# Kernel tuning notes

Measured on AMD Instinct MI355X. Metric: run time of the kernel, lower is better.

Reference implementation:

```python
import jax, jax.numpy as jnp
import numpy as np

N_CODE, PC = 127, 63
LENGTH = N_CODE + PC          # 190
D_MODEL, D_STATE, D_CONV, EXPAND = 512, 16, 4, 2
D_INNER = EXPAND * D_MODEL    # 1024
DT_RANK = (D_MODEL + 15) // 16  # 32
BATCH = 16


def _build_mask(pcm):
    # faithful translation of build_mask(code)
    L = N_CODE + PC
    mask = np.eye(L, dtype=np.float64)
    for r in range(PC):
        idx = np.where(pcm[r] > 0)[0]
        for jj in idx:
            for kk in idx:
                if jj != kk:
                    mask[jj, kk] += 1
                    mask[kk, jj] += 1
                    mask[N_CODE + r, jj] += 1
                    mask[jj, N_CODE + r] += 1
    return mask > 0


def setup_inputs() -> dict:
    rng = np.random.default_rng(0)
    # LDPC-like sparse parity-check matrix, row weight 6
    pcm = np.zeros((PC, N_CODE), np.int32)
    for r in range(PC):
        pcm[r, rng.choice(N_CODE, 6, replace=False)] = 1
    pc_mask = jnp.asarray(_build_mask(pcm))

    def w(shape, fan_in):
        return jnp.asarray((rng.standard_normal(shape) / np.sqrt(fan_in)).astype(np.float32))

    inp = {
        "x": jnp.asarray(rng.standard_normal((BATCH, LENGTH, D_MODEL)).astype(np.float32)),
        "pc_mask": pc_mask,
        # masked resize linears (torch Linear: y = x @ W.T + b)
        "in_resize_w": w((LENGTH, D_MODEL), D_MODEL),
        "in_resize_b": jnp.zeros((LENGTH,), jnp.float32),
        "in_reset_w": w((D_MODEL, LENGTH), LENGTH),
        "in_reset_b": jnp.zeros((D_MODEL,), jnp.float32),
        "out_resize_w": w((LENGTH, D_MODEL), D_MODEL),
        "out_resize_b": jnp.zeros((LENGTH,), jnp.float32),
        "out_reset_w": w((D_MODEL, LENGTH), LENGTH),
        "out_reset_b": jnp.zeros((D_MODEL,), jnp.float32),
        # Mamba block params
        "in_proj_w": w((2 * D_INNER, D_MODEL), D_MODEL),
        "conv_w": w((D_INNER, D_CONV), D_CONV),          # depthwise conv kernels
        "conv_b": jnp.zeros((D_INNER,), jnp.float32),
        "x_proj_w": w((DT_RANK + 2 * D_STATE, D_INNER), D_INNER),
        "dt_proj_w": w((D_INNER, DT_RANK), DT_RANK),
        "dt_proj_b": jnp.full((D_INNER,), -4.6, jnp.float32),  # softplus ~ 0.01
        "A_log": jnp.log(jnp.tile(jnp.arange(1, D_STATE + 1, dtype=jnp.float32), (D_INNER, 1))),
        "D": jnp.ones((D_INNER,), jnp.float32),
        "out_proj_w": w((D_MODEL, D_INNER), D_INNER),
        # LayerNorm over (length, d_model)
        "norm_w": jnp.ones((LENGTH, D_MODEL), jnp.float32),
        "norm_b": jnp.zeros((LENGTH, D_MODEL), jnp.float32),
    }
    return inp


def _forward(x, pc_mask, in_resize_w, in_resize_b, in_reset_w, in_reset_b,
             out_resize_w, out_resize_b, out_reset_w, out_reset_b,
             in_proj_w, conv_w, conv_b, x_proj_w, dt_proj_w, dt_proj_b,
             A_log, D, out_proj_w, norm_w, norm_b):
    dt_rank = dt_proj_w.shape[1]
    d_state = A_log.shape[1]
    d_conv = conv_w.shape[1]

    def mamba(h):
        # h: [B, L, d_model]
        xz = h @ in_proj_w.T                       # [B, L, 2*d_inner]
        xc, z = jnp.split(xz, 2, axis=-1)
        # depthwise causal conv along L
        xt = xc.transpose(0, 2, 1)                 # [B, d_inner, L]
        xt = jax.lax.conv_general_dilated(
            xt, conv_w[:, None, :], (1,), [(d_conv - 1, 0)],
            dimension_numbers=("NCH", "OIH", "NCH"),
            feature_group_count=xt.shape[1])
        xc = jax.nn.silu((xt + conv_b[None, :, None]).transpose(0, 2, 1))  # [B,L,di]
        x_dbl = xc @ x_proj_w.T                    # [B, L, dt_rank+2*ds]
        dt = jax.nn.softplus(x_dbl[..., :dt_rank] @ dt_proj_w.T + dt_proj_b)
        Bm = x_dbl[..., dt_rank:dt_rank + d_state]  # [B, L, ds]
        Cm = x_dbl[..., dt_rank + d_state:]         # [B, L, ds]
        A = -jnp.exp(A_log)                         # [di, ds]
        dA = jnp.exp(dt[..., None] * A)             # [B, L, di, ds]
        dBu = (dt * xc)[..., None] * Bm[:, :, None, :]

        def step(hst, inp):
            a, b = inp
            hst = a * hst + b
            return hst, hst

        h0 = jnp.zeros((dA.shape[0], dA.shape[2], dA.shape[3]), dA.dtype)
        _, hs = jax.lax.scan(step, h0, (dA.transpose(1, 0, 2, 3), dBu.transpose(1, 0, 2, 3)))
        y = jnp.einsum("lbds,bls->bld", hs, Cm) + xc * D
        return (y * jax.nn.silu(z)) @ out_proj_w.T  # [B, L, d_model]

    m = pc_mask.astype(x.dtype)
    h = (x @ in_resize_w.T + in_resize_b) * m[0, 0]
    h = (h @ in_reset_w.T + in_reset_b) * x
    o = mamba(h) + jnp.flip(mamba(jnp.flip(h, 1)), 1)  # bidirectional scan
    o = (o @ out_resize_w.T + out_resize_b) * m        # [B,L,L] * [L,L]
    o = (o @ out_reset_w.T + out_reset_b) * x
    # LayerNorm over last two dims (length, d_model)
    t = jnp.tanh(x)
    mu = jnp.mean(t, axis=(-2, -1), keepdims=True)
    var = jnp.var(t, axis=(-2, -1), keepdims=True)
    out = (t - mu) * jax.lax.rsqrt(var + 1e-5) * norm_w + norm_b
    # original module returns only `out`; `o` is also returned here to keep the
    # (otherwise dead) bidirectional selective-scan path observable.
    return out, o


def reference(x, pc_mask, in_resize_w, in_resize_b, in_reset_w, in_reset_b,
              out_resize_w, out_resize_b, out_reset_w, out_reset_b,
              in_proj_w, conv_w, conv_b, x_proj_w, dt_proj_w, dt_proj_b,
              A_log, D, out_proj_w, norm_w, norm_b):
    return _forward(x, pc_mask, in_resize_w, in_resize_b, in_reset_w, in_reset_b,
                    out_resize_w, out_resize_b, out_reset_w, out_reset_b,
                    in_proj_w, conv_w, conv_b, x_proj_w, dt_proj_w, dt_proj_b,
                    A_log, D, out_proj_w, norm_w, norm_b)
```

## Files before the change

kernel.cpp:

```cpp
#include <hip/hip_runtime.h>
#include <hip/hip_bf16.h>

#define B_    16
#define L_    190
#define LP_   192
#define DM_   512
#define DI_   1024
#define LB_   3040
#define RT_   6080
#define LBDI_ 3112960

typedef __attribute__((ext_vector_type(8))) short bf16x8;
typedef __attribute__((ext_vector_type(4))) float f32x4;
typedef __attribute__((ext_vector_type(4))) unsigned short u16x4;

typedef const __attribute__((address_space(1))) void gvoid;
typedef __attribute__((address_space(3))) void lvoid;
#define LOAD_LDS16(g, l) __builtin_amdgcn_global_load_lds((gvoid*)(g), (lvoid*)(l), 16, 0, 0)

__device__ __forceinline__ float siluf(float v) { return v / (1.f + __expf(-v)); }
__device__ __forceinline__ float softplusf(float v) {
  return v > 0.f ? v + log1pf(__expf(-v)) : log1pf(__expf(v));
}
__device__ __forceinline__ float bf2f(unsigned short u) {
  unsigned int w = (unsigned int)u << 16; return __builtin_bit_cast(float, w);
}

__global__ __launch_bounds__(256) void mask_convert(const void* __restrict__ pcm,
                                                    float* __restrict__ maskf,
                                                    const float* __restrict__ irb,
                                                    const float* __restrict__ orb,
                                                    float* __restrict__ b_inrs,
                                                    float* __restrict__ b_outrs)
{
  __shared__ int votes[3];
  if (threadIdx.x < 3) votes[threadIdx.x] = 0;
  __syncthreads();
  if (threadIdx.x < 48) {
    int idx = threadIdx.x * 191;
    const unsigned char* p8  = (const unsigned char*)pcm;
    const unsigned int*  p32 = (const unsigned int*)pcm;
    if (p8[idx] == 1) atomicAdd(&votes[0], 1);
    unsigned int v = p32[idx];
    if (v == 1u)          atomicAdd(&votes[1], 1);
    if (v == 0x3f800000u) atomicAdd(&votes[2], 1);
  }
  __syncthreads();
  int mode = (votes[0] >= 48) ? 0 : (votes[1] >= 48 ? 1 : (votes[2] >= 48 ? 2 : 0));
  int i = blockIdx.x * 256 + threadIdx.x;
  if (i < L_ * LP_) {
    int r = i / LP_, c = i % LP_;
    float v = 0.f;
    if (c < L_) {
      int s = r * L_ + c;
      if (mode == 0)      v = ((const unsigned char*)pcm)[s] ? 1.f : 0.f;
      else if (mode == 1) v = ((const int*)pcm)[s] ? 1.f : 0.f;
      else                v = ((const float*)pcm)[s];
    }
    maskf[i] = v;
  }
  if (blockIdx.x == 0 && threadIdx.x < LP_) {
    b_inrs[threadIdx.x]  = (threadIdx.x < L_) ? irb[threadIdx.x] : 0.f;
    b_outrs[threadIdx.x] = (threadIdx.x < L_) ? orb[threadIdx.x] : 0.f;
  }
}

struct Cvt2 { const float* src; __hip_bfloat16* dst; int R, C, Rp, Cp; };
struct CvtPack2 { Cvt2 d[9]; };

__global__ __launch_bounds__(256) void cvt_all2(CvtPack2 p)
{
  Cvt2 D = p.d[blockIdx.y];
  int n = D.Rp * D.Cp;
  if (D.C == D.Cp) {
    int nsrc = D.R * D.C;
    for (int i4 = (blockIdx.x * 256 + threadIdx.x) * 4; i4 < n; i4 += gridDim.x * 256 * 4) {
      __hip_bfloat16 o[4];
      if (i4 + 3 < nsrc) {
        f32x4 v = *(const f32x4*)(D.src + i4);
        #pragma unroll
        for (int q = 0; q < 4; ++q) o[q] = __float2bfloat16(v[q]);
      } else {
        #pragma unroll
        for (int q = 0; q < 4; ++q) { int i = i4 + q; o[q] = __float2bfloat16(i < nsrc ? D.src[i] : 0.f); }
      }
      *(u16x4*)(D.dst + i4) = *(u16x4*)o;
    }
  } else {
    for (int i = blockIdx.x * 256 + threadIdx.x; i < n; i += gridDim.x * 256) {
      int r = i / D.Cp, c = i - r * D.Cp;
      float v = (r < D.R && c < D.C) ? D.src[(size_t)r * D.C + c] : 0.f;
      D.dst[i] = __float2bfloat16(v);
    }
  }
}

template<int EPI, bool OF32, bool OBF>
__global__ __launch_bounds__(256) void gemm128(
    const __hip_bfloat16* __restrict__ A, int lda, int M,
    const __hip_bfloat16* __restrict__ Bw, int Brows,
    const float* __restrict__ bias, const float* __restrict__ aux,
    float* __restrict__ Cf, __hip_bfloat16* __restrict__ Cb,
    int N, int K)
{
  __shared__ bf16x8 SA[2][512];
  __shared__ bf16x8 SB[2][512];
  const int tid = threadIdx.x;
  const int wave = tid >> 6, lane = tid & 63;
  const int m0 = blockIdx.y * 128, n0 = blockIdx.x * 128;
  const int wm = (wave >> 1) * 64, wn = (wave & 1) * 64;
  const int l15 = lane & 15, lkb = lane >> 4;

  f32x4 acc[4][4] = {};

  auto stage = [&](int bsel, int k0) {
    #pragma unroll
    for (int it = 0; it < 2; ++it) {
      int c = it * 256 + tid;
      int row = c & 127, kb = c >> 7;
      int ar = m0 + row; ar = ar < M ? ar : M - 1;
      const __hip_bfloat16* ga = A + (size_t)ar * lda + (k0 + kb * 8);
      LOAD_LDS16(ga, &SA[bsel][it * 256 + wave * 64]);
      int br = n0 + row; br = br < Brows ? br : Brows - 1;
      const __hip_bfloat16* gb = Bw + (size_t)br * K + (k0 + kb * 8);
      LOAD_LDS16(gb, &SB[bsel][it * 256 + wave * 64]);
    }
  };

  const int nk = K >> 5;
  stage(0, 0);
  __syncthreads();
  int buf = 0;
  for (int kt = 0; kt < nk; ++kt) {
    if (kt + 1 < nk) stage(buf ^ 1, (kt + 1) * 32);
    bf16x8 af[4], bq[4];
    #pragma unroll
    for (int f = 0; f < 4; ++f) {
      af[f] = SA[buf][lkb * 128 + wm + f * 16 + l15];
      bq[f] = SB[buf][lkb * 128 + wn + f * 16 + l15];
    }
    #pragma unroll
    for (int i = 0; i < 4; ++i)
      #pragma unroll
      for (int j = 0; j < 4; ++j)
        acc[i][j] = __builtin_amdgcn_mfma_f32_16x16x32_bf16(af[i], bq[j], acc[i][j], 0, 0, 0);
    __syncthreads();
    buf ^= 1;
  }

  #pragma unroll
  for (int i = 0; i < 4; ++i) {
    int r0 = m0 + wm + i * 16 + (lkb << 2);
    #pragma unroll
    for (int j = 0; j < 4; ++j) {
      int col = n0 + wn + j * 16 + l15;
      if (col >= N) continue;
      #pragma unroll
      for (int r = 0; r < 4; ++r) {
        int row = r0 + r;
        if (row >= M) continue;
        float v = acc[i][j][r];
        if (EPI >= 1) v += bias[col];
        if (EPI == 2) v *= aux[(size_t)row * N + col];
        if (EPI == 3) v = softplusf(v);
        if (EPI == 4) v *= aux[(size_t)(row % L_) * N + col];
        if (OF32) Cf[(size_t)row * N + col] = v;
        if (OBF)  Cb[(size_t)row * N + col] = __float2bfloat16(v);
      }
    }
  }
}

template<int EPI, bool OF32, bool OBF>
__global__ __launch_bounds__(256) void gemm64(
    const __hip_bfloat16* __restrict__ A, int lda, int M,
    const __hip_bfloat16* __restrict__ Bw, int Brows,
    const float* __restrict__ bias, const float* __restrict__ aux,
    float* __restrict__ Cf, __hip_bfloat16* __restrict__ Cb,
    int N, int K)
{
  __shared__ bf16x8 SA[2][256];
  __shared__ bf16x8 SB[2][256];
  const int tid = threadIdx.x;
  const int wave = tid >> 6, lane = tid & 63;
  const int m0 = blockIdx.y * 64, n0 = blockIdx.x * 64;
  const int wm = (wave >> 1) * 32, wn = (wave & 1) * 32;
  const int l15 = lane & 15, lkb = lane >> 4;

  f32x4 acc[2][2] = {};

  auto stage = [&](int bsel, int k0) {
    int row = tid & 63, kb = tid >> 6;
    int ar = m0 + row; ar = ar < M ? ar : M - 1;
    const __hip_bfloat16* ga = A + (size_t)ar * lda + (k0 + kb * 8);
    LOAD_LDS16(ga, &SA[bsel][wave * 64]);
    int br = n0 + row; br = br < Brows ? br : Brows - 1;
    const __hip_bfloat16* gb = Bw + (size_t)br * K + (k0 + kb * 8);
    LOAD_LDS16(gb, &SB[bsel][wave * 64]);
  };

  const int nk = K >> 5;
  stage(0, 0);
  __syncthreads();
  int buf = 0;
  for (int kt = 0; kt < nk; ++kt) {
    if (kt + 1 < nk) stage(buf ^ 1, (kt + 1) * 32);
    bf16x8 af[2], bq[2];
    #pragma unroll
    for (int f = 0; f < 2; ++f) {
      af[f] = SA[buf][lkb * 64 + wm + f * 16 + l15];
      bq[f] = SB[buf][lkb * 64 + wn + f * 16 + l15];
    }
    #pragma unroll
    for (int i = 0; i < 2; ++i)
      #pragma unroll
      for (int j = 0; j < 2; ++j)
        acc[i][j] = __builtin_amdgcn_mfma_f32_16x16x32_bf16(af[i], bq[j], acc[i][j], 0, 0, 0);
    __syncthreads();
    buf ^= 1;
  }

  #pragma unroll
  for (int i = 0; i < 2; ++i) {
    int r0 = m0 + wm + i * 16 + (lkb << 2);
    #pragma unroll
    for (int j = 0; j < 2; ++j) {
      int col = n0 + wn + j * 16 + l15;
      if (col >= N) continue;
      #pragma unroll
      for (int r = 0; r < 4; ++r) {
        int row = r0 + r;
        if (row >= M) continue;
        float v = acc[i][j][r];
        if (EPI >= 1) v += bias[col];
        if (EPI == 2) v *= aux[(size_t)row * N + col];
        if (EPI == 3) v = softplusf(v);
        if (EPI == 4) v *= aux[(size_t)(row % L_) * N + col];
        if (OF32) Cf[(size_t)row * N + col] = v;
        if (OBF)  Cb[(size_t)row * N + col] = __float2bfloat16(v);
      }
    }
  }
}

__global__ __launch_bounds__(256) void conv_silu(
    const __hip_bfloat16* __restrict__ xz, const float* __restrict__ w,
    const float* __restrict__ cb, __hip_bfloat16* __restrict__ xcbf)
{
  int t = blockIdx.x * 256 + threadIdx.x;
  int c4 = (t & (DI_ / 4 - 1)) * 4;
  int bl = t >> 8;
  int l = bl % L_;
  int b = bl / L_;
  const __hip_bfloat16* base = xz + (size_t)b * L_ * (2 * DI_) + c4;
  float xr[7][4];
  #pragma unroll
  for (int j = 0; j < 7; ++j) {
    int gl = l + j - 3;
    if (gl >= 0 && gl < L_) {
      u16x4 v = *(const u16x4*)(base + (size_t)gl * (2 * DI_));
      #pragma unroll
      for (int q = 0; q < 4; ++q) xr[j][q] = bf2f(v[q]);
    } else {
      #pragma unroll
      for (int q = 0; q < 4; ++q) xr[j][q] = 0.f;
    }
  }
  __hip_bfloat16 of[4], ob[4];
  #pragma unroll
  for (int q = 0; q < 4; ++q) {
    int c = c4 + q;
    float w0 = w[c * 4], w1 = w[c * 4 + 1], w2 = w[c * 4 + 2], w3 = w[c * 4 + 3];
    float bias = cb[c];
    float sf = fmaf(w0, xr[0][q], fmaf(w1, xr[1][q], fmaf(w2, xr[2][q], fmaf(w3, xr[3][q], bias))));
    float sb = fmaf(w0, xr[6][q], fmaf(w1, xr[5][q], fmaf(w2, xr[4][q], fmaf(w3, xr[3][q], bias))));
    of[q] = __float2bfloat16(siluf(sf));
    ob[q] = __float2bfloat16(siluf(sb));
  }
  size_t o = (size_t)bl * DI_ + c4;
  *(u16x4*)(xcbf + o)         = *(u16x4*)of;
  *(u16x4*)(xcbf + LBDI_ + o) = *(u16x4*)ob;
}

#define SCT_ 24
#define HS_  17
__global__ __launch_bounds__(256) void scan_v9(
    const __hip_bfloat16* __restrict__ dtb,
    const float* __restrict__ xd,
    const __hip_bfloat16* __restrict__ xc,
    const float* __restrict__ A_log, const float* __restrict__ Dv,
    __hip_bfloat16* __restrict__ y)
{
  __shared__ float sH[256 * HS_];
  __shared__ float sS[256];

  const int tid   = threadIdx.x;
  const int dl    = tid & 31;
  const int chunk = tid >> 5;
  const int dglob = blockIdx.x * 32 + dl;
  const int b     = blockIdx.y;
  const int dir   = blockIdx.z;
  const int rowbase = dir * LB_ + b * L_;
  const unsigned short* xcu = (const unsigned short*)xc;
  const unsigned short* dtu = (const unsigned short*)dtb;
  const float* Arow = A_log + dglob * 16;

  const float A0 = -__expf(Arow[0]);
  bool fast = true;
  #pragma unroll
  for (int s = 1; s < 16; ++s) {
    float As = -__expf(Arow[s]);
    fast = fast && (fabsf(As - (float)(s + 1) * A0) <= 1e-4f * (float)(s + 1));
  }
  const float Dd = Dv[dglob];

  const int cstart = chunk * SCT_;
  const int clen = (cstart + SCT_ <= L_) ? SCT_ : (L_ > cstart ? L_ - cstart : 0);

  auto powers = [&](float e1, float* ep) {
    ep[0] = e1;
    #pragma unroll
    for (int s = 1; s < 16; ++s) ep[s] = ep[(s - 1) >> 1] * ep[s >> 1];
  };

  float h[16];
  #pragma unroll
  for (int s = 0; s < 16; ++s) h[s] = 0.f;
  float dsum = 0.f;
  for (int k = 0; k < clen; ++k) {
    int l   = cstart + k;
    int pos = dir ? (L_ - 1 - l) : l;
    size_t grow = (size_t)(rowbase + pos);
    float dtv = bf2f(dtu[grow * DI_ + dglob]);
    float xcv = bf2f(xcu[grow * DI_ + dglob]);
    float du  = dtv * xcv;
    dsum += dtv;
    const float* brow = xd + grow * 64;
    f32x4 bq0 = *(const f32x4*)(brow + 32);
    f32x4 bq1 = *(const f32x4*)(brow + 36);
    f32x4 bq2 = *(const f32x4*)(brow + 40);
    f32x4 bq3 = *(const f32x4*)(brow + 44);
    float ep[16];
    if (fast) {
      powers(__expf(dtv * A0), ep);
    } else {
      #pragma unroll
      for (int s = 0; s < 16; ++s) ep[s] = __expf(dtv * -__expf(Arow[s]));
    }
    #pragma unroll
    for (int s = 0; s < 16; ++s) {
      float Bv = (s < 4) ? bq0[s & 3] : (s < 8) ? bq1[s & 3] : (s < 12) ? bq2[s & 3] : bq3[s & 3];
      h[s] = fmaf(ep[s], h[s], du * Bv);
    }
  }
  {
    float* hr = sH + tid * HS_;
    #pragma unroll
    for (int s = 0; s < 16; ++s) hr[s] = h[s];
    sS[tid] = dsum;
  }
  __syncthreads();

  float hin[16];
  #pragma unroll
  for (int s = 0; s < 16; ++s) hin[s] = 0.f;
  for (int c = 0; c < chunk; ++c) {
    float S = sS[c * 32 + dl];
    const float* hp = sH + (c * 32 + dl) * HS_;
    float ep[16];
    if (fast) {
      powers(__expf(A0 * S), ep);
    } else {
      #pragma unroll
      for (int s = 0; s < 16; ++s) ep[s] = __expf(-__expf(Arow[s]) * S);
    }
    #pragma unroll
    for (int s = 0; s < 16; ++s)
      hin[s] = fmaf(ep[s], hin[s], hp[s]);
  }

  #pragma unroll
  for (int s = 0; s < 16; ++s) h[s] = hin[s];
  for (int k = 0; k < clen; ++k) {
    int l   = cstart + k;
    int pos = dir ? (L_ - 1 - l) : l;
    size_t grow = (size_t)(rowbase + pos);
    float dtv = bf2f(dtu[grow * DI_ + dglob]);
    float xcv = bf2f(xcu[grow * DI_ + dglob]);
    float du  = dtv * xcv;
    const float* brow = xd + grow * 64;
    f32x4 bq0 = *(const f32x4*)(brow + 32);
    f32x4 bq1 = *(const f32x4*)(brow + 36);
    f32x4 bq2 = *(const f32x4*)(brow + 40);
    f32x4 bq3 = *(const f32x4*)(brow + 44);
    f32x4 cq0 = *(const f32x4*)(brow + 48);
    f32x4 cq1 = *(const f32x4*)(brow + 52);
    f32x4 cq2 = *(const f32x4*)(brow + 56);
    f32x4 cq3 = *(const f32x4*)(brow + 60);
    float ep[16];
    if (fast) {
      powers(__expf(dtv * A0), ep);
    } else {
      #pragma unroll
      for (int s = 0; s < 16; ++s) ep[s] = __expf(dtv * -__expf(Arow[s]));
    }
    float acc = 0.f;
    #pragma unroll
    for (int s = 0; s < 16; ++s) {
      float Bv = (s < 4) ? bq0[s & 3] : (s < 8) ? bq1[s & 3] : (s < 12) ? bq2[s & 3] : bq3[s & 3];
      float Cv = (s < 4) ? cq0[s & 3] : (s < 8) ? cq1[s & 3] : (s < 12) ? cq2[s & 3] : cq3[s & 3];
      h[s] = fmaf(ep[s], h[s], du * Bv);
      acc  = fmaf(h[s], Cv, acc);
    }
    y[grow * DI_ + dglob] = __float2bfloat16(fmaf(xcv, Dd, acc));
  }
}

__global__ __launch_bounds__(256) void combine_yz(
    const __hip_bfloat16* __restrict__ y, const __hip_bfloat16* __restrict__ xz,
    __hip_bfloat16* __restrict__ yz)
{
  int t = blockIdx.x * 256 + threadIdx.x;
  int c4 = (t & (DI_ / 4 - 1)) * 4;
  int rowi = t >> 8;
  size_t o = (size_t)rowi * DI_ + c4;
  u16x4 yf = *(const u16x4*)(y + o);
  u16x4 yb = *(const u16x4*)(y + LBDI_ + o);
  u16x4 zv = *(const u16x4*)(xz + (size_t)rowi * (2 * DI_) + DI_ + c4);
  __hip_bfloat16 out[4];
  #pragma unroll
  for (int q = 0; q < 4; ++q) {
    float z = bf2f(zv[q]);
    out[q] = __float2bfloat16((bf2f(yf[q]) + bf2f(yb[q])) * siluf(z));
  }
  *(u16x4*)(yz + o) = *(u16x4*)out;
}

__global__ __launch_bounds__(256) void ln_partial(const float* __restrict__ x,
                                                  float* __restrict__ partials)
{
  int b = blockIdx.y, ch = blockIdx.x;
  const float* xb = x + (size_t)b * (L_ * DM_);
  int lo = ch * 12160, hi = lo + 12160;
  float s = 0.f, s2 = 0.f;
  for (int i = lo + threadIdx.x; i < hi; i += 256) {
    float t = tanhf(xb[i]);
    s += t; s2 = fmaf(t, t, s2);
  }
  #pragma unroll
  for (int off = 32; off > 0; off >>= 1) { s += __shfl_down(s, off); s2 += __shfl_down(s2, off); }
  __shared__ float rs[4], rs2[4];
  int wid = threadIdx.x >> 6, lane = threadIdx.x & 63;
  if (lane == 0) { rs[wid] = s; rs2[wid] = s2; }
  __syncthreads();
  if (threadIdx.x == 0) {
    partials[(b * 8 + ch) * 2 + 0] = rs[0] + rs[1] + rs[2] + rs[3];
    partials[(b * 8 + ch) * 2 + 1] = rs2[0] + rs2[1] + rs2[2] + rs2[3];
  }
}

__global__ __launch_bounds__(256) void ln_final(const float* __restrict__ x,
    const float* __restrict__ partials,
    const float* __restrict__ nw, const float* __restrict__ nb,
    float* __restrict__ out)
{
  int b = blockIdx.y, ch = blockIdx.x;
  float S = 0.f, S2 = 0.f;
  #pragma unroll
  for (int i = 0; i < 8; ++i) { S += partials[(b * 8 + i) * 2 + 0]; S2 += partials[(b * 8 + i) * 2 + 1]; }
  const float inv = 1.f / (float)(L_ * DM_);
  float mu = S * inv;
  float var = S2 * inv - mu * mu;
  float r = rsqrtf(var + 1e-5f);
  const float* xb = x + (size_t)b * (L_ * DM_);
  float* ob = out + (size_t)b * (L_ * DM_);
  int lo = ch * 12160, hi = lo + 12160;
  for (int i = lo + threadIdx.x; i < hi; i += 256) {
    float t = tanhf(xb[i]);
    ob[i] = fmaf((t - mu) * r, nw[i], nb[i]);
  }
}

extern "C" void kernel_launch(void* const* d_in, const int* in_sizes, int n_in,
                              void* d_out, int out_size, void* d_ws, size_t ws_size,
                              hipStream_t stream)
{
  const float* x            = (const float*)d_in[0];
  const void*  pc_mask      = d_in[1];
  const float* in_resize_w  = (const float*)d_in[2];
  const float* in_resize_b  = (const float*)d_in[3];
  const float* in_reset_w   = (const float*)d_in[4];
  const float* in_reset_b   = (const float*)d_in[5];
  const float* out_resize_w = (const float*)d_in[6];
  const float* out_resize_b = (const float*)d_in[7];
  const float* out_reset_w  = (const float*)d_in[8];
  const float* out_reset_b  = (const float*)d_in[9];
  const float* in_proj_w    = (const float*)d_in[10];
  const float* conv_w       = (const float*)d_in[11];
  const float* conv_b       = (const float*)d_in[12];
  const float* x_proj_w     = (const float*)d_in[13];
  const float* dt_proj_w    = (const float*)d_in[14];
  const float* dt_proj_b    = (const float*)d_in[15];
  const float* A_log        = (const float*)d_in[16];
  const float* Dv           = (const float*)d_in[17];
  const float* out_proj_w   = (const float*)d_in[18];
  const float* norm_w       = (const float*)d_in[19];
  const float* norm_b       = (const float*)d_in[20];

  float* W = (float*)d_ws;
  float* maskf    = W + 0;
  float* b_inrs   = W + 36480;
  float* b_outrs  = W + 36672;
  float* xd       = W + 36864;
  float* partials = W + 425984;
  __hip_bfloat16* BF = (__hip_bfloat16*)(W + 426240);
  __hip_bfloat16* w_inrs  = BF + 0;
  __hip_bfloat16* w_inrt  = BF + 98304;
  __hip_bfloat16* w_inpj  = BF + 196608;
  __hip_bfloat16* w_xpj   = BF + 1245184;
  __hip_bfloat16* w_dtpj  = BF + 1310720;
  __hip_bfloat16* w_outpj = BF + 1343488;
  __hip_bfloat16* w_outrs = BF + 1867776;
  __hip_bfloat16* w_outrt = BF + 1966080;
  __hip_bfloat16* x_bf    = BF + 2064384;
  __hip_bfloat16* h1_bf   = BF + 3620864;
  __hip_bfloat16* h_bf    = BF + 4204544;
  __hip_bfloat16* xz_bf   = BF + 5761024;
  __hip_bfloat16* xc_bf   = BF + 11986944;
  __hip_bfloat16* y_bf    = BF + 18212864;
  __hip_bfloat16* xd_bf   = BF + 24438784;
  __hip_bfloat16* dt_bf   = BF + 24827904;
  __hip_bfloat16* yz_bf   = BF + 31053824;
  __hip_bfloat16* o_pre   = BF + 34166784;
  __hip_bfloat16* o2_bf   = BF + 35723264;

  float* out_ln = (float*)d_out;
  float* out_o  = (float*)d_out + (size_t)LB_ * DM_;

  dim3 blk(256);

  mask_convert<<<dim3(143), blk, 0, stream>>>(pc_mask, maskf, in_resize_b, out_resize_b, b_inrs, b_outrs);

  CvtPack2 P;
  P.d[0] = Cvt2{ x,            x_bf,    3040, 512, 3040, 512 };
  P.d[1] = Cvt2{ in_resize_w,  w_inrs,  190, 512, 192, 512 };
  P.d[2] = Cvt2{ in_reset_w,   w_inrt,  512, 190, 512, 192 };
  P.d[3] = Cvt2{ in_proj_w,    w_inpj,  2048, 512, 2048, 512 };
  P.d[4] = Cvt2{ x_proj_w,     w_xpj,   64, 1024, 64, 1024 };
  P.d[5] = Cvt2{ dt_proj_w,    w_dtpj,  1024, 32, 1024, 32 };
  P.d[6] = Cvt2{ out_proj_w,   w_outpj, 512, 1024, 512, 1024 };
  P.d[7] = Cvt2{ out_resize_w, w_outrs, 190, 512, 192, 512 };
  P.d[8] = Cvt2{ out_reset_w,  w_outrt, 512, 190, 512, 192 };
  cvt_all2<<<dim3(256, 9), blk, 0, stream>>>(P);

  gemm64<1,false,true><<<dim3(3,48), blk, 0, stream>>>(x_bf, 512, 3040, w_inrs, 192, b_inrs, nullptr, nullptr, h1_bf, LP_, 512);
  gemm64<2,false,true><<<dim3(8,48), blk, 0, stream>>>(h1_bf, LP_, 3040, w_inrt, 512, in_reset_b, x, nullptr, h_bf, 512, LP_);
  gemm128<0,false,true><<<dim3(16,24), blk, 0, stream>>>(h_bf, 512, 3040, w_inpj, 2048, nullptr, nullptr, nullptr, xz_bf, 2048, 512);
  conv_silu<<<dim3(LBDI_/1024), blk, 0, stream>>>(xz_bf, conv_w, conv_b, xc_bf);
  gemm64<0,true,true><<<dim3(1,95), blk, 0, stream>>>(xc_bf, 1024, 6080, w_xpj, 64, nullptr, nullptr, xd, xd_bf, 64, 1024);
  gemm64<3,false,true><<<dim3(16,95), blk, 0, stream>>>(xd_bf, 64, 6080, w_dtpj, 1024, dt_proj_b, nullptr, nullptr, dt_bf, 1024, 32);
  scan_v9<<<dim3(32, 16, 2), blk, 0, stream>>>(dt_bf, xd, xc_bf, A_log, Dv, y_bf);
  combine_yz<<<dim3(LBDI_/1024), blk, 0, stream>>>(y_bf, xz_bf, yz_bf);
  gemm64<0,false,true><<<dim3(8,48), blk, 0, stream>>>(yz_bf, 1024, 3040, w_outpj, 512, nullptr, nullptr, nullptr, o_pre, 512, 1024);
  gemm64<4,false,true><<<dim3(3,48), blk, 0, stream>>>(o_pre, 512, 3040, w_outrs, 192, b_outrs, maskf, nullptr, o2_bf, LP_, 512);
  gemm64<2,true,false><<<dim3(8,48), blk, 0, stream>>>(o2_bf, LP_, 3040, w_outrt, 512, out_reset_b, x, out_o, nullptr, 512, LP_);
  dim3 lgrid(8, B_);
  ln_partial<<<lgrid, blk, 0, stream>>>(x, partials);
  ln_final<<<lgrid, blk, 0, stream>>>(x, partials, norm_w, norm_b, out_ln);
}
```

Before: 263.2 us.

## Fuse mask conversion into cvt, fold yz combine into out_proj GEMM, cache scan inputs

The mask conversion kernel is merged into the weight conversion launch as an extra grid slice, and the combine_yz kernel is folded into a new out_proj GEMM that computes (y_fwd+y_bwd)*silu(z) while staging its A tile. The scan's second pass now reuses dt/xc values packed into registers from the first pass instead of reloading them, with fully unrolled fixed-length loops. This removes two launches and an intermediate yz buffer round trip. The cost is more register pressure in the scan and redundant silu work in the GEMM, since each A element is recomputed by every N-block.

```diff
diff --git a/kernel.cpp b/kernel.cpp
--- a/kernel.cpp
+++ b/kernel.cpp
@@ -26,50 +26,46 @@
   unsigned int w = (unsigned int)u << 16; return __builtin_bit_cast(float, w);
 }
 
-__global__ __launch_bounds__(256) void mask_convert(const void* __restrict__ pcm,
-                                                    float* __restrict__ maskf,
-                                                    const float* __restrict__ irb,
-                                                    const float* __restrict__ orb,
-                                                    float* __restrict__ b_inrs,
-                                                    float* __restrict__ b_outrs)
-{
-  __shared__ int votes[3];
-  if (threadIdx.x < 3) votes[threadIdx.x] = 0;
-  __syncthreads();
-  if (threadIdx.x < 48) {
-    int idx = threadIdx.x * 191;
-    const unsigned char* p8  = (const unsigned char*)pcm;
-    const unsigned int*  p32 = (const unsigned int*)pcm;
-    if (p8[idx] == 1) atomicAdd(&votes[0], 1);
-    unsigned int v = p32[idx];
-    if (v == 1u)          atomicAdd(&votes[1], 1);
-    if (v == 0x3f800000u) atomicAdd(&votes[2], 1);
-  }
-  __syncthreads();
-  int mode = (votes[0] >= 48) ? 0 : (votes[1] >= 48 ? 1 : (votes[2] >= 48 ? 2 : 0));
-  int i = blockIdx.x * 256 + threadIdx.x;
-  if (i < L_ * LP_) {
-    int r = i / LP_, c = i % LP_;
-    float v = 0.f;
-    if (c < L_) {
-      int s = r * L_ + c;
-      if (mode == 0)      v = ((const unsigned char*)pcm)[s] ? 1.f : 0.f;
-      else if (mode == 1) v = ((const int*)pcm)[s] ? 1.f : 0.f;
-      else                v = ((const float*)pcm)[s];
-    }
-    maskf[i] = v;
-  }
-  if (blockIdx.x == 0 && threadIdx.x < LP_) {
-    b_inrs[threadIdx.x]  = (threadIdx.x < L_) ? irb[threadIdx.x] : 0.f;
-    b_outrs[threadIdx.x] = (threadIdx.x < L_) ? orb[threadIdx.x] : 0.f;
-  }
-}
-
 struct Cvt2 { const float* src; __hip_bfloat16* dst; int R, C, Rp, Cp; };
 struct CvtPack2 { Cvt2 d[9]; };
 
-__global__ __launch_bounds__(256) void cvt_all2(CvtPack2 p)
-{
+__global__ __launch_bounds__(256) void cvt_all3(CvtPack2 p,
+    const void* __restrict__ pcm, float* __restrict__ maskf,
+    const float* __restrict__ irb, const float* __restrict__ orb,
+    float* __restrict__ b_inrs, float* __restrict__ b_outrs)
+{
+  if (blockIdx.y == 9) {
+    __shared__ int votes[3];
+    if (threadIdx.x < 3) votes[threadIdx.x] = 0;
+    __syncthreads();
+    if (threadIdx.x < 48) {
+      int idx = threadIdx.x * 191;
+      const unsigned char* p8  = (const unsigned char*)pcm;
+      const unsigned int*  p32 = (const unsigned int*)pcm;
+      if (p8[idx] == 1) atomicAdd(&votes[0], 1);
+      unsigned int v = p32[idx];
+      if (v == 1u)          atomicAdd(&votes[1], 1);
+      if (v == 0x3f800000u) atomicAdd(&votes[2], 1);
+    }
+    __syncthreads();
+    int mode = (votes[0] >= 48) ? 0 : (votes[1] >= 48 ? 1 : (votes[2] >= 48 ? 2 : 0));
+    for (int i = blockIdx.x * 256 + threadIdx.x; i < L_ * LP_; i += gridDim.x * 256) {
+      int r = i / LP_, c = i % LP_;
+      float v = 0.f;
+      if (c < L_) {
+        int s = r * L_ + c;
+        if (mode == 0)      v = ((const unsigned char*)pcm)[s] ? 1.f : 0.f;
+        else if (mode == 1) v = ((const int*)pcm)[s] ? 1.f : 0.f;
+        else                v = ((const float*)pcm)[s];
+      }
+      maskf[i] = v;
+    }
+    if (blockIdx.x == 0 && threadIdx.x < LP_) {
+      b_inrs[threadIdx.x]  = (threadIdx.x < L_) ? irb[threadIdx.x] : 0.f;
+      b_outrs[threadIdx.x] = (threadIdx.x < L_) ? orb[threadIdx.x] : 0.f;
+    }
+    return;
+  }
   Cvt2 D = p.d[blockIdx.y];
   int n = D.Rp * D.Cp;
   if (D.C == D.Cp) {
@@ -243,6 +239,86 @@
   }
 }
 
+__global__ __launch_bounds__(256) void gemm64_yz(
+    const __hip_bfloat16* __restrict__ Y,
+    const __hip_bfloat16* __restrict__ Xz,
+    const __hip_bfloat16* __restrict__ Bw,
+    __hip_bfloat16* __restrict__ Cb,
+    int M, int N, int K)
+{
+  __shared__ bf16x8 SA[2][256];
+  __shared__ bf16x8 SB[2][256];
+  const int tid = threadIdx.x;
+  const int wave = tid >> 6, lane = tid & 63;
+  const int m0 = blockIdx.y * 64, n0 = blockIdx.x * 64;
+  const int wm = (wave >> 1) * 32, wn = (wave & 1) * 32;
+  const int l15 = lane & 15, lkb = lane >> 4;
+
+  f32x4 acc[2][2] = {};
+
+  auto stage = [&](int bsel, int k0) {
+    int row = tid & 63, kb = tid >> 6;
+    int ar = m0 + row; ar = ar < M ? ar : M - 1;
+    size_t o = (size_t)ar * DI_ + (k0 + kb * 8);
+    u16x4 f0 = *(const u16x4*)(Y + o);
+    u16x4 f1 = *(const u16x4*)(Y + o + 4);
+    u16x4 g0 = *(const u16x4*)(Y + LBDI_ + o);
+    u16x4 g1 = *(const u16x4*)(Y + LBDI_ + o + 4);
+    size_t zo = (size_t)ar * (2 * DI_) + DI_ + (k0 + kb * 8);
+    u16x4 z0 = *(const u16x4*)(Xz + zo);
+    u16x4 z1 = *(const u16x4*)(Xz + zo + 4);
+    unsigned short av[8];
+    #pragma unroll
+    for (int q = 0; q < 4; ++q) {
+      float v = (bf2f(f0[q]) + bf2f(g0[q])) * siluf(bf2f(z0[q]));
+      av[q] = __bfloat16_as_ushort(__float2bfloat16(v));
+      float w = (bf2f(f1[q]) + bf2f(g1[q])) * siluf(bf2f(z1[q]));
+      av[q + 4] = __bfloat16_as_ushort(__float2bfloat16(w));
+    }
+    SA[bsel][wave * 64 + row] = *(bf16x8*)av;
+    int br = n0 + row; br = br < N ? br : N - 1;
+    const __hip_bfloat16* gb = Bw + (size_t)br * K + (k0 + kb * 8);
+    LOAD_LDS16(gb, &SB[bsel][wave * 64]);
+  };
+
+  const int nk = K >> 5;
+  stage(0, 0);
+  __syncthreads();
+  int buf = 0;
+  for (int kt = 0; kt < nk; ++kt) {
+    if (kt + 1 < nk) stage(buf ^ 1, (kt + 1) * 32);
+    bf16x8 af[2], bq[2];
+    #pragma unroll
+    for (int f = 0; f < 2; ++f) {
+      af[f] = SA[buf][lkb * 64 + wm + f * 16 + l15];
+      bq[f] = SB[buf][lkb * 64 + wn + f * 16 + l15];
+    }
+    #pragma unroll
+    for (int i = 0; i < 2; ++i)
+      #pragma unroll
+      for (int j = 0; j < 2; ++j)
+        acc[i][j] = __builtin_amdgcn_mfma_f32_16x16x32_bf16(af[i], bq[j], acc[i][j], 0, 0, 0);
+    __syncthreads();
+    buf ^= 1;
+  }
+
+  #pragma unroll
+  for (int i = 0; i < 2; ++i) {
+    int r0 = m0 + wm + i * 16 + (lkb << 2);
+    #pragma unroll
+    for (int j = 0; j < 2; ++j) {
+      int col = n0 + wn + j * 16 + l15;
+      if (col >= N) continue;
+      #pragma unroll
+      for (int r = 0; r < 4; ++r) {
+        int row = r0 + r;
+        if (row >= M) continue;
+        Cb[(size_t)row * N + col] = __float2bfloat16(acc[i][j][r]);
+      }
+    }
+  }
+}
+
 __global__ __launch_bounds__(256) void conv_silu(
     const __hip_bfloat16* __restrict__ xz, const float* __restrict__ w,
     const float* __restrict__ cb, __hip_bfloat16* __restrict__ xcbf)
@@ -284,7 +360,7 @@
 
 #define SCT_ 24
 #define HS_  17
-__global__ __launch_bounds__(256) void scan_v9(
+__global__ __launch_bounds__(256) void scan_v10(
     const __hip_bfloat16* __restrict__ dtb,
     const float* __restrict__ xd,
     const __hip_bfloat16* __restrict__ xc,
@@ -313,9 +389,7 @@
     fast = fast && (fabsf(As - (float)(s + 1) * A0) <= 1e-4f * (float)(s + 1));
   }
   const float Dd = Dv[dglob];
-
   const int cstart = chunk * SCT_;
-  const int clen = (cstart + SCT_ <= L_) ? SCT_ : (L_ > cstart ? L_ - cstart : 0);
 
   auto powers = [&](float e1, float* ep) {
     ep[0] = e1;
@@ -323,16 +397,23 @@
     for (int s = 1; s < 16; ++s) ep[s] = ep[(s - 1) >> 1] * ep[s >> 1];
   };
 
+  unsigned int pk[SCT_];
   float h[16];
   #pragma unroll
   for (int s = 0; s < 16; ++s) h[s] = 0.f;
   float dsum = 0.f;
-  for (int k = 0; k < clen; ++k) {
-    int l   = cstart + k;
+  #pragma unroll
+  for (int k = 0; k < SCT_; ++k) {
+    int l = cstart + k;
+    bool valid = l < L_;
     int pos = dir ? (L_ - 1 - l) : l;
+    pos = valid ? pos : 0;
     size_t grow = (size_t)(rowbase + pos);
-    float dtv = bf2f(dtu[grow * DI_ + dglob]);
-    float xcv = bf2f(xcu[grow * DI_ + dglob]);
+    unsigned short du16 = valid ? dtu[grow * DI_ + dglob] : (unsigned short)0;
+    unsigned short xu16 = valid ? xcu[grow * DI_ + dglob] : (unsigned short)0;
+    pk[k] = ((unsigned int)du16 << 16) | xu16;
+    float dtv = bf2f(du16);
+    float xcv = bf2f(xu16);
     float du  = dtv * xcv;
     dsum += dtv;
     const float* brow = xd + grow * 64;
@@ -381,12 +462,15 @@
 
   #pragma unroll
   for (int s = 0; s < 16; ++s) h[s] = hin[s];
-  for (int k = 0; k < clen; ++k) {
-    int l   = cstart + k;
+  #pragma unroll
+  for (int k = 0; k < SCT_; ++k) {
+    int l = cstart + k;
+    bool valid = l < L_;
     int pos = dir ? (L_ - 1 - l) : l;
+    pos = valid ? pos : 0;
     size_t grow = (size_t)(rowbase + pos);
-    float dtv = bf2f(dtu[grow * DI_ + dglob]);
-    float xcv = bf2f(xcu[grow * DI_ + dglob]);
+    float dtv = bf2f((unsigned short)(pk[k] >> 16));
+    float xcv = bf2f((unsigned short)(pk[k] & 0xFFFFu));
     float du  = dtv * xcv;
     const float* brow = xd + grow * 64;
     f32x4 bq0 = *(const f32x4*)(brow + 32);
@@ -412,28 +496,9 @@
       h[s] = fmaf(ep[s], h[s], du * Bv);
       acc  = fmaf(h[s], Cv, acc);
     }
-    y[grow * DI_ + dglob] = __float2bfloat16(fmaf(xcv, Dd, acc));
-  }
-}
-
-__global__ __launch_bounds__(256) void combine_yz(
-    const __hip_bfloat16* __restrict__ y, const __hip_bfloat16* __restrict__ xz,
-    __hip_bfloat16* __restrict__ yz)
-{
-  int t = blockIdx.x * 256 + threadIdx.x;
-  int c4 = (t & (DI_ / 4 - 1)) * 4;
-  int rowi = t >> 8;
-  size_t o = (size_t)rowi * DI_ + c4;
-  u16x4 yf = *(const u16x4*)(y + o);
-  u16x4 yb = *(const u16x4*)(y + LBDI_ + o);
-  u16x4 zv = *(const u16x4*)(xz + (size_t)rowi * (2 * DI_) + DI_ + c4);
-  __hip_bfloat16 out[4];
-  #pragma unroll
-  for (int q = 0; q < 4; ++q) {
-    float z = bf2f(zv[q]);
-    out[q] = __float2bfloat16((bf2f(yf[q]) + bf2f(yb[q])) * siluf(z));
-  }
-  *(u16x4*)(yz + o) = *(u16x4*)out;
+    if (valid)
+      y[grow * DI_ + dglob] = __float2bfloat16(fmaf(xcv, Dd, acc));
+  }
 }
 
 __global__ __launch_bounds__(256) void ln_partial(const float* __restrict__ x,
@@ -530,16 +595,13 @@
   __hip_bfloat16* y_bf    = BF + 18212864;
   __hip_bfloat16* xd_bf   = BF + 24438784;
   __hip_bfloat16* dt_bf   = BF + 24827904;
-  __hip_bfloat16* yz_bf   = BF + 31053824;
-  __hip_bfloat16* o_pre   = BF + 34166784;
-  __hip_bfloat16* o2_bf   = BF + 35723264;
+  __hip_bfloat16* o_pre   = BF + 31053824;
+  __hip_bfloat16* o2_bf   = BF + 32610304;
 
   float* out_ln = (float*)d_out;
   float* out_o  = (float*)d_out + (size_t)LB_ * DM_;
 
   dim3 blk(256);
-
-  mask_convert<<<dim3(143), blk, 0, stream>>>(pc_mask, maskf, in_resize_b, out_resize_b, b_inrs, b_outrs);
 
   CvtPack2 P;
   P.d[0] = Cvt2{ x,            x_bf,    3040, 512, 3040, 512 };
@@ -551,7 +613,8 @@
   P.d[6] = Cvt2{ out_proj_w,   w_outpj, 512, 1024, 512, 1024 };
   P.d[7] = Cvt2{ out_resize_w, w_outrs, 190, 512, 192, 512 };
   P.d[8] = Cvt2{ out_reset_w,  w_outrt, 512, 190, 512, 192 };
-  cvt_all2<<<dim3(256, 9), blk, 0, stream>>>(P);
+  cvt_all3<<<dim3(256, 10), blk, 0, stream>>>(P, pc_mask, maskf,
+      in_resize_b, out_resize_b, b_inrs, b_outrs);
 
   gemm64<1,false,true><<<dim3(3,48), blk, 0, stream>>>(x_bf, 512, 3040, w_inrs, 192, b_inrs, nullptr, nullptr, h1_bf, LP_, 512);
   gemm64<2,false,true><<<dim3(8,48), blk, 0, stream>>>(h1_bf, LP_, 3040, w_inrt, 512, in_reset_b, x, nullptr, h_bf, 512, LP_);
@@ -559,9 +622,8 @@
   conv_silu<<<dim3(LBDI_/1024), blk, 0, stream>>>(xz_bf, conv_w, conv_b, xc_bf);
   gemm64<0,true,true><<<dim3(1,95), blk, 0, stream>>>(xc_bf, 1024, 6080, w_xpj, 64, nullptr, nullptr, xd, xd_bf, 64, 1024);
   gemm64<3,false,true><<<dim3(16,95), blk, 0, stream>>>(xd_bf, 64, 6080, w_dtpj, 1024, dt_proj_b, nullptr, nullptr, dt_bf, 1024, 32);
-  scan_v9<<<dim3(32, 16, 2), blk, 0, stream>>>(dt_bf, xd, xc_bf, A_log, Dv, y_bf);
-  combine_yz<<<dim3(LBDI_/1024), blk, 0, stream>>>(y_bf, xz_bf, yz_bf);
-  gemm64<0,false,true><<<dim3(8,48), blk, 0, stream>>>(yz_bf, 1024, 3040, w_outpj, 512, nullptr, nullptr, nullptr, o_pre, 512, 1024);
+  scan_v10<<<dim3(32, 16, 2), blk, 0, stream>>>(dt_bf, xd, xc_bf, A_log, Dv, y_bf);
+  gemm64_yz<<<dim3(8,48), blk, 0, stream>>>(y_bf, xz_bf, w_outpj, o_pre, 3040, 512, 1024);
   gemm64<4,false,true><<<dim3(3,48), blk, 0, stream>>>(o_pre, 512, 3040, w_outrs, 192, b_outrs, maskf, nullptr, o2_bf, LP_, 512);
   gemm64<2,true,false><<<dim3(8,48), blk, 0, stream>>>(o2_bf, LP_, 3040, w_outrt, 512, out_reset_b, x, out_o, nullptr, 512, LP_);
   dim3 lgrid(8, B_);
```

New measurement: 578.0 us. +119.6%, slower.
